# Kernel optimization log

Hardware: AMD Instinct MI355X
Metric: run time of the kernel (lower is better)

Reference implementation:

```python
import jax, jax.numpy as jnp
import numpy as np

B, H, W = 8, 512, 512          # batch, detector grid
M_PER_B = 32768
N = B * M_PER_B
C_IN, C_OUT, RED = 64, 128, 4
EPS = 1e-5


def setup_inputs() -> dict:
    key = jax.random.key(0)
    ks = jax.random.split(key, 8)
    # unique active-site indices per batch (permutation of flat grid cells)
    rng = np.random.default_rng(0)
    rows = []
    for b in range(B):
        flat = rng.permutation(H * W)[:M_PER_B]
        y, x = flat // W, flat % W
        rows.append(np.stack([np.full(M_PER_B, b), y, x], axis=1))
    indices = jnp.asarray(np.concatenate(rows, 0), dtype=jnp.int32)  # [N,3]

    feats = jax.random.normal(ks[0], (N, C_IN), jnp.float32)
    s1 = 1.0 / np.sqrt(9 * C_IN)
    s2 = 1.0 / np.sqrt(9 * C_OUT)
    return {
        "feats": feats,
        "indices": indices,
        "bn1_g": jnp.ones((C_IN,), jnp.float32),
        "bn1_b": jnp.zeros((C_IN,), jnp.float32),
        "w1": jax.random.normal(ks[1], (9, C_IN, C_OUT), jnp.float32) * s1,
        "bn2_g": jnp.ones((C_OUT,), jnp.float32),
        "bn2_b": jnp.zeros((C_OUT,), jnp.float32),
        "w2": jax.random.normal(ks[2], (9, C_OUT, C_OUT), jnp.float32) * s2,
        "fc1_w": jax.random.normal(ks[3], (C_OUT // RED, C_OUT), jnp.float32) / np.sqrt(C_OUT),
        "fc1_b": jnp.zeros((C_OUT // RED,), jnp.float32),
        "fc2_w": jax.random.normal(ks[4], (C_OUT, C_OUT // RED), jnp.float32) / np.sqrt(C_OUT // RED),
        "fc2_b": jnp.zeros((C_OUT,), jnp.float32),
        "w_skip": jax.random.normal(ks[5], (C_IN, C_OUT), jnp.float32) / np.sqrt(C_IN),
    }


def build_rulebook(indices):
    """Neighbor point-ids for each 3x3 offset. Returns ids [N,9], mask [N,9]."""
    n = indices.shape[0]
    b, y, x = indices[:, 0], indices[:, 1], indices[:, 2]
    grid = jnp.full((B, H, W), -1, jnp.int32).at[b, y, x].set(
        jnp.arange(n, dtype=jnp.int32))
    ids, masks = [], []
    for dy in (-1, 0, 1):
        for dx in (-1, 0, 1):
            ny, nx = y + dy, x + dx
            inb = (ny >= 0) & (ny < H) & (nx >= 0) & (nx < W)
            nid = grid[b, jnp.clip(ny, 0, H - 1), jnp.clip(nx, 0, W - 1)]
            m = inb & (nid >= 0)
            ids.append(jnp.where(m, nid, 0))
            masks.append(m)
    return jnp.stack(ids, 1), jnp.stack(masks, 1)


def subm_conv(f, nbr_ids, nbr_mask, w):
    """Submanifold 3x3 conv: gather-GEMM-scatter over active sites."""
    out = jnp.zeros((f.shape[0], w.shape[2]), f.dtype)
    for k in range(w.shape[0]):  # fixed 9 kernel offsets
        g = jnp.where(nbr_mask[:, k:k + 1], f[nbr_ids[:, k]], 0.0)
        out = out + g @ w[k]
    return out


def batchnorm(x, g, b):
    m = jnp.mean(x, 0)
    v = jnp.var(x, 0)  # biased, matches torch BN training normalization
    return (x - m) * jax.lax.rsqrt(v + EPS) * g + b


def reference(feats, indices, bn1_g, bn1_b, w1, bn2_g, bn2_b, w2,
              fc1_w, fc1_b, fc2_w, fc2_b, w_skip):
    nbr_ids, nbr_mask = build_rulebook(indices)  # shared indice_key rulebook
    bidx = indices[:, 0]

    out = jax.nn.relu(batchnorm(feats, bn1_g, bn1_b))
    out = subm_conv(out, nbr_ids, nbr_mask, w1)
    out = jax.nn.relu(batchnorm(out, bn2_g, bn2_b))
    out = subm_conv(out, nbr_ids, nbr_mask, w2)

    # SE: scatter-mean pool per event, FC-ReLU-FC-Sigmoid, per-site rescale
    pooled = jax.ops.segment_sum(out, bidx, num_segments=B)
    counts = jax.ops.segment_sum(jnp.ones((out.shape[0], 1), out.dtype), bidx,
                                 num_segments=B)
    pooled = pooled / jnp.clip(counts, 1.0, None)
    se = jax.nn.sigmoid(jax.nn.relu(pooled @ fc1_w.T + fc1_b) @ fc2_w.T + fc2_b)
    out = out * se[bidx]

    identity = feats @ w_skip  # 1x1 subm conv skip (in_ch != out_ch)
    return out + identity
```

## Files before the change

### kernel.cpp

```cpp
#include <hip/hip_runtime.h>
#include <math.h>

#define NPTS 262144
#define BB 8
#define HH 512
#define WW 512
#define EPSV 1e-5f

typedef short short8v __attribute__((ext_vector_type(8)));
typedef short short4v __attribute__((ext_vector_type(4)));
typedef float float4v __attribute__((ext_vector_type(4)));
typedef unsigned short ushort;
typedef ushort ushort8v __attribute__((ext_vector_type(8)));

static __device__ __forceinline__ ushort f2bf(float f) {
  union { float f; unsigned u; } v;
  v.f = f;
  unsigned r = v.u + 0x7fffu + ((v.u >> 16) & 1u);
  return (ushort)(r >> 16);
}

static __device__ __forceinline__ float bf2f(ushort h) {
  union { unsigned u; float f; } v;
  v.u = ((unsigned)h) << 16;
  return v.f;
}


__global__ __launch_bounds__(256) void k_scatter(const int* __restrict__ idx,
                                                 int* __restrict__ grid) {
  int i = blockIdx.x * 256 + threadIdx.x;
  int b = idx[i * 3 + 0], y = idx[i * 3 + 1], x = idx[i * 3 + 2];
  grid[(b * HH + y) * WW + x] = i;
}

__global__ __launch_bounds__(256) void k_rulebook(const int* __restrict__ idx,
                                                  const int* __restrict__ grid,
                                                  int* __restrict__ nbr) {
  int i = blockIdx.x * 256 + threadIdx.x;
  int b = idx[i * 3 + 0], y = idx[i * 3 + 1], x = idx[i * 3 + 2];
  int t = 0;
  #pragma unroll
  for (int dy = -1; dy <= 1; ++dy) {
    #pragma unroll
    for (int dx = -1; dx <= 1; ++dx) {
      int ny = y + dy, nx = x + dx;
      int v = -1;
      if (ny >= 0 && ny < HH && nx >= 0 && nx < WW)
        v = grid[(b * HH + ny) * WW + nx];
      nbr[i * 9 + t] = v;
      ++t;
    }
  }
}


__global__ __launch_bounds__(256) void k_stats64(const float* __restrict__ x,
                                                 float* __restrict__ sum,
                                                 float* __restrict__ ssum) {
  __shared__ float red_s[4][64];
  __shared__ float red_q[4][64];
  const int tid = threadIdx.x;
  const int lane = tid & 63;
  const int wave = tid >> 6;
  const int c4 = lane & 15;
  const int rq = lane >> 4;
  long long base = (long long)blockIdx.x * 256;
  float s0 = 0.f, s1 = 0.f, s2 = 0.f, s3 = 0.f;
  float q0 = 0.f, q1 = 0.f, q2 = 0.f, q3 = 0.f;
  for (int r = wave * 4 + rq; r < 256; r += 16) {
    float4 v = *(const float4*)(x + (base + r) * 64 + c4 * 4);
    s0 += v.x; s1 += v.y; s2 += v.z; s3 += v.w;
    q0 += v.x * v.x; q1 += v.y * v.y; q2 += v.z * v.z; q3 += v.w * v.w;
  }
  s0 += __shfl_xor(s0, 16, 64); s0 += __shfl_xor(s0, 32, 64);
  s1 += __shfl_xor(s1, 16, 64); s1 += __shfl_xor(s1, 32, 64);
  s2 += __shfl_xor(s2, 16, 64); s2 += __shfl_xor(s2, 32, 64);
  s3 += __shfl_xor(s3, 16, 64); s3 += __shfl_xor(s3, 32, 64);
  q0 += __shfl_xor(q0, 16, 64); q0 += __shfl_xor(q0, 32, 64);
  q1 += __shfl_xor(q1, 16, 64); q1 += __shfl_xor(q1, 32, 64);
  q2 += __shfl_xor(q2, 16, 64); q2 += __shfl_xor(q2, 32, 64);
  q3 += __shfl_xor(q3, 16, 64); q3 += __shfl_xor(q3, 32, 64);
  if (rq == 0) {
    red_s[wave][c4 * 4 + 0] = s0; red_s[wave][c4 * 4 + 1] = s1;
    red_s[wave][c4 * 4 + 2] = s2; red_s[wave][c4 * 4 + 3] = s3;
    red_q[wave][c4 * 4 + 0] = q0; red_q[wave][c4 * 4 + 1] = q1;
    red_q[wave][c4 * 4 + 2] = q2; red_q[wave][c4 * 4 + 3] = q3;
  }
  __syncthreads();
  if (tid < 64) {
    float ts = red_s[0][tid] + red_s[1][tid] + red_s[2][tid] + red_s[3][tid];
    float tq = red_q[0][tid] + red_q[1][tid] + red_q[2][tid] + red_q[3][tid];
    atomicAdd(&sum[tid], ts);
    atomicAdd(&ssum[tid], tq);
  }
}

template <int CI>
__global__ void k_finalize(const float* __restrict__ sum, const float* __restrict__ ssum,
                           const float* __restrict__ gam, const float* __restrict__ bet,
                           float* __restrict__ sc, float* __restrict__ sh) {
  int c = threadIdx.x;
  if (c < CI) {
    float m = sum[c] * (1.f / NPTS);
    float v = ssum[c] * (1.f / NPTS) - m * m;
    float s = gam[c] * rsqrtf(v + EPSV);
    sc[c] = s;
    sh[c] = bet[c] - m * s;
  }
}


__global__ __launch_bounds__(256) void k_wprep(const float* __restrict__ w,
                                               ushort* __restrict__ wt,
                                               int taps, int ci) {
  int i = blockIdx.x * 256 + threadIdx.x;
  int total = taps * ci * 128;
  if (i < total) {
    int t = i / (ci * 128);
    int rem = i - t * ci * 128;
    int c = rem >> 7;
    int o = rem & 127;
    wt[((size_t)t * 128 + o) * ci + c] = f2bf(w[i]);
  }
}


template <typename SrcT, typename DstT, int CI, int TAPS, bool ACT, int EPI>
__global__ __launch_bounds__(256) void k_conv(const SrcT* __restrict__ src,
                                              const float* __restrict__ scale,
                                              const float* __restrict__ shift,
                                              const int* __restrict__ nbr,
                                              const ushort* __restrict__ wt,
                                              DstT* __restrict__ dst,
                                              float* __restrict__ e0,
                                              float* __restrict__ e1) {
  constexpr int SA = CI + 8;
  __shared__ ushort As[128 * SA];
  __shared__ ushort Bs[128 * SA];
  __shared__ float s_sc[CI], s_sh[CI];

  const int tid = threadIdx.x;
  const int base = blockIdx.x * 128;
  const int lane = tid & 63;
  const int wave = tid >> 6;
  const int wm = wave & 1, wn = wave >> 1;
  const int m_base = wm * 64, n_base = wn * 64;
  const int fm = lane & 15;
  const int fq = lane >> 4;

  if constexpr (ACT) {
    for (int c = tid; c < CI; c += 256) {
      s_sc[c] = scale[c];
      s_sh[c] = shift[c];
    }
  }
  __syncthreads();

  float4v acc[4][4];
  #pragma unroll
  for (int i = 0; i < 4; ++i)
    #pragma unroll
    for (int j = 0; j < 4; ++j) acc[i][j] = (float4v){0.f, 0.f, 0.f, 0.f};

  const int srow_i = tid >> 1;
  const int shalf = tid & 1;
  const int c0 = shalf * (CI / 2);

  for (int k = 0; k < TAPS; ++k) {
    if (k) __syncthreads();

    int nid;
    if constexpr (TAPS == 1) {
      nid = base + srow_i;
    } else {
      nid = nbr[(base + srow_i) * 9 + k];
    }
    ushort* arow = &As[srow_i * SA + c0];
    if (nid >= 0) {
      const SrcT* gsrc = src + (size_t)nid * CI + c0;
      if constexpr (sizeof(SrcT) == 4) {
        #pragma unroll
        for (int j = 0; j < CI / 2; j += 4) {
          float4 v = *(const float4*)((const float*)gsrc + j);
          if constexpr (ACT) {
            int c = c0 + j;
            v.x = fmaxf(v.x * s_sc[c + 0] + s_sh[c + 0], 0.f);
            v.y = fmaxf(v.y * s_sc[c + 1] + s_sh[c + 1], 0.f);
            v.z = fmaxf(v.z * s_sc[c + 2] + s_sh[c + 2], 0.f);
            v.w = fmaxf(v.w * s_sc[c + 3] + s_sh[c + 3], 0.f);
          }
          short4v o = {(short)f2bf(v.x), (short)f2bf(v.y), (short)f2bf(v.z), (short)f2bf(v.w)};
          *(short4v*)(arow + j) = o;
        }
      } else {
        #pragma unroll
        for (int j = 0; j < CI / 2; j += 8) {
          ushort8v raw = *(const ushort8v*)((const ushort*)gsrc + j);
          short8v o;
          #pragma unroll
          for (int e = 0; e < 8; ++e) {
            float f = bf2f(raw[e]);
            if constexpr (ACT) {
              int c = c0 + j + e;
              f = fmaxf(f * s_sc[c] + s_sh[c], 0.f);
            }
            o[e] = (short)f2bf(f);
          }
          *(short8v*)(arow + j) = o;
        }
      }
    } else {
      #pragma unroll
      for (int j = 0; j < CI / 2; j += 4)
        *(short4v*)(arow + j) = (short4v){0, 0, 0, 0};
    }

    {
      const ushort* wrow = wt + ((size_t)k * 128 + srow_i) * CI + c0;
      ushort* brow = &Bs[srow_i * SA + c0];
      #pragma unroll
      for (int j = 0; j < CI / 2; j += 8)
        *(uint4*)(brow + j) = *(const uint4*)(wrow + j);
    }
    __syncthreads();

    #pragma unroll
    for (int kc = 0; kc < CI / 32; ++kc) {
      short8v af[4], bf[4];
      #pragma unroll
      for (int mi = 0; mi < 4; ++mi)
        af[mi] = *(const short8v*)(&As[(m_base + mi * 16 + fm) * SA + kc * 32 + fq * 8]);
      #pragma unroll
      for (int ni = 0; ni < 4; ++ni)
        bf[ni] = *(const short8v*)(&Bs[(n_base + ni * 16 + fm) * SA + kc * 32 + fq * 8]);
      #pragma unroll
      for (int mi = 0; mi < 4; ++mi)
        #pragma unroll
        for (int ni = 0; ni < 4; ++ni)
          acc[mi][ni] = __builtin_amdgcn_mfma_f32_16x16x32_bf16(af[mi], bf[ni], acc[mi][ni], 0, 0, 0);
    }
  }

  float es[4], ess[4];
  if constexpr (EPI) {
    #pragma unroll
    for (int ni = 0; ni < 4; ++ni) { es[ni] = 0.f; ess[ni] = 0.f; }
  }
  #pragma unroll
  for (int mi = 0; mi < 4; ++mi) {
    #pragma unroll
    for (int ni = 0; ni < 4; ++ni) {
      int pt = base + m_base + mi * 16 + fq * 4;
      int co = n_base + ni * 16 + fm;
      float4v c = acc[mi][ni];
      #pragma unroll
      for (int r = 0; r < 4; ++r) {
        if constexpr (sizeof(DstT) == 4) {
          ((float*)dst)[(size_t)(pt + r) * 128 + co] = c[r];
          if constexpr (EPI == 2) es[ni] += c[r];
        } else {
          ushort h = f2bf(c[r]);
          ((ushort*)dst)[(size_t)(pt + r) * 128 + co] = h;
          if constexpr (EPI == 1) {
            float v = bf2f(h);
            es[ni] += v;
            ess[ni] += v * v;
          }
        }
      }
    }
  }

  if constexpr (EPI) {
    #pragma unroll
    for (int ni = 0; ni < 4; ++ni) {
      float s = es[ni];
      s += __shfl_xor(s, 16, 64);
      s += __shfl_xor(s, 32, 64);
      float q = 0.f;
      if constexpr (EPI == 1) {
        q = ess[ni];
        q += __shfl_xor(q, 16, 64);
        q += __shfl_xor(q, 32, 64);
      }
      if (fq == 0) {
        int co = n_base + ni * 16 + fm;
        if constexpr (EPI == 1) {
          atomicAdd(&e0[co], s);
          atomicAdd(&e1[co], q);
        } else {
          int b = base >> 15;
          atomicAdd(&e0[b * 128 + co], s);
        }
      }
    }
  }
}


__global__ __launch_bounds__(256) void k_se(const float* __restrict__ pooled,
                                            const float* __restrict__ fc1w,
                                            const float* __restrict__ fc1b,
                                            const float* __restrict__ fc2w,
                                            const float* __restrict__ fc2b,
                                            float* __restrict__ se) {
  __shared__ float h[8][32];
  int tid = threadIdx.x;
  int b = tid >> 5, j = tid & 31;
  float s = fc1b[j];
  for (int c = 0; c < 128; ++c)
    s += pooled[b * 128 + c] * (1.f / 32768.f) * fc1w[j * 128 + c];
  h[b][j] = fmaxf(s, 0.f);
  __syncthreads();
  for (int t = tid; t < 1024; t += 256) {
    int bb = t >> 7, c = t & 127;
    float s2 = fc2b[c];
    #pragma unroll
    for (int jj = 0; jj < 32; ++jj) s2 += h[bb][jj] * fc2w[c * 32 + jj];
    se[t] = 1.f / (1.f + expf(-s2));
  }
}

__global__ __launch_bounds__(256) void k_final(float* __restrict__ out,
                                               const ushort* __restrict__ id,
                                               const float* __restrict__ se) {
  long long i = ((long long)blockIdx.x * 256 + threadIdx.x) * 4;
  int co = (int)(i & 127);
  long long rowi = i >> 7;
  int b = (int)(rowi >> 15);
  float4 o = *(const float4*)(out + i);
  ushort dh[4];
  *(uint2*)dh = *(const uint2*)(id + i);
  float4 s = *(const float4*)(se + b * 128 + co);
  o.x = o.x * s.x + bf2f(dh[0]);
  o.y = o.y * s.y + bf2f(dh[1]);
  o.z = o.z * s.z + bf2f(dh[2]);
  o.w = o.w * s.w + bf2f(dh[3]);
  *(float4*)(out + i) = o;
}


extern "C" void kernel_launch(void* const* d_in, const int* in_sizes, int n_in,
                              void* d_out, int out_size, void* d_ws, size_t ws_size,
                              hipStream_t stream) {
  const float* feats = (const float*)d_in[0];
  const int* indices = (const int*)d_in[1];
  const float* bn1_g = (const float*)d_in[2];
  const float* bn1_b = (const float*)d_in[3];
  const float* w1    = (const float*)d_in[4];
  const float* bn2_g = (const float*)d_in[5];
  const float* bn2_b = (const float*)d_in[6];
  const float* w2    = (const float*)d_in[7];
  const float* fc1w  = (const float*)d_in[8];
  const float* fc1b  = (const float*)d_in[9];
  const float* fc2w  = (const float*)d_in[10];
  const float* fc2b  = (const float*)d_in[11];
  const float* wskip = (const float*)d_in[12];
  float* out = (float*)d_out;

  char* p = (char*)d_ws;
  int* nbr = (int*)p;       p += (size_t)NPTS * 9 * 4;
  float* stats = (float*)p; p += 4096 * 4;
  ushort* wt1 = (ushort*)p; p += (size_t)9 * 128 * 64 * 2;
  ushort* wt2 = (ushort*)p; p += (size_t)9 * 128 * 128 * 2;
  ushort* wts = (ushort*)p; p += (size_t)128 * 64 * 2;
  p = (char*)(((size_t)p + 255) & ~(size_t)255);
  int* grid_i = (int*)p;
  ushort* out1 = (ushort*)p;

  float* sum1 = stats, *ss1 = stats + 64, *sc1 = stats + 128, *sh1 = stats + 192;
  float* sum2 = stats + 256, *ss2 = stats + 384, *sc2 = stats + 512, *sh2 = stats + 640;
  float* pooled = stats + 768;
  float* se = stats + 1792;

  hipMemsetAsync(grid_i, 0xFF, (size_t)BB * HH * WW * 4, stream);
  hipMemsetAsync(stats, 0, 4096 * 4, stream);

  k_scatter<<<NPTS / 256, 256, 0, stream>>>(indices, grid_i);
  k_rulebook<<<NPTS / 256, 256, 0, stream>>>(indices, grid_i, nbr);

  k_wprep<<<(9 * 64 * 128 + 255) / 256, 256, 0, stream>>>(w1, wt1, 9, 64);
  k_wprep<<<(9 * 128 * 128 + 255) / 256, 256, 0, stream>>>(w2, wt2, 9, 128);
  k_wprep<<<(64 * 128 + 255) / 256, 256, 0, stream>>>(wskip, wts, 1, 64);

  k_stats64<<<NPTS / 256, 256, 0, stream>>>(feats, sum1, ss1);
  k_finalize<64><<<1, 64, 0, stream>>>(sum1, ss1, bn1_g, bn1_b, sc1, sh1);

  k_conv<float, ushort, 64, 9, true, 1><<<NPTS / 128, 256, 0, stream>>>(
      feats, sc1, sh1, nbr, wt1, out1, sum2, ss2);

  k_finalize<128><<<1, 128, 0, stream>>>(sum2, ss2, bn2_g, bn2_b, sc2, sh2);

  k_conv<ushort, float, 128, 9, true, 2><<<NPTS / 128, 256, 0, stream>>>(
      out1, sc2, sh2, nbr, wt2, out, pooled, nullptr);

  k_conv<float, ushort, 64, 1, false, 0><<<NPTS / 128, 256, 0, stream>>>(
      feats, nullptr, nullptr, nullptr, wts, out1, nullptr, nullptr);

  k_se<<<1, 256, 0, stream>>>(pooled, fc1w, fc1b, fc2w, fc2b, se);
  k_final<<<NPTS * 128 / 1024, 256, 0, stream>>>(out, out1, se);
}
```

Before: 675.7 us.

## Pre-normalize activations to bf16 and gather directly into MFMA fragments

Adds standalone BN+ReLU kernels that write pre-normalized bf16 activations, so the convolution no longer normalizes and converts each neighbor on every tap. A new direct-gather conv kernel loads A fragments from global memory straight into MFMA registers, with no LDS staging and no __syncthreads. The rulebook is transposed to tap-major so neighbor-id loads are coalesced. This costs two extra elementwise passes and scattered 16-byte gathers that may miss cache. A fallback path keeps the old kernels when the workspace is too small.

```diff
diff --git a/kernel.cpp b/kernel.cpp
--- a/kernel.cpp
+++ b/kernel.cpp
@@ -36,7 +36,7 @@
 
 __global__ __launch_bounds__(256) void k_rulebook(const int* __restrict__ idx,
                                                   const int* __restrict__ grid,
-                                                  int* __restrict__ nbr) {
+                                                  int* __restrict__ nbrT) {
   int i = blockIdx.x * 256 + threadIdx.x;
   int b = idx[i * 3 + 0], y = idx[i * 3 + 1], x = idx[i * 3 + 2];
   int t = 0;
@@ -48,7 +48,7 @@
       int v = -1;
       if (ny >= 0 && ny < HH && nx >= 0 && nx < WW)
         v = grid[(b * HH + ny) * WW + nx];
-      nbr[i * 9 + t] = v;
+      nbrT[(size_t)t * NPTS + i] = v;
       ++t;
     }
   }
@@ -111,6 +111,53 @@
 }
 
 
+__global__ __launch_bounds__(256) void k_norm1(const float* __restrict__ x,
+                                               const float* __restrict__ sc,
+                                               const float* __restrict__ sh,
+                                               ushort* __restrict__ y) {
+  long long i = ((long long)blockIdx.x * 256 + threadIdx.x) * 8;
+  int c = (int)(i & 63);
+  float4 a = *(const float4*)(x + i);
+  float4 b = *(const float4*)(x + i + 4);
+  float4 s0 = *(const float4*)(sc + c);
+  float4 s1 = *(const float4*)(sc + c + 4);
+  float4 h0 = *(const float4*)(sh + c);
+  float4 h1 = *(const float4*)(sh + c + 4);
+  ushort8v o;
+  o[0] = f2bf(fmaxf(a.x * s0.x + h0.x, 0.f));
+  o[1] = f2bf(fmaxf(a.y * s0.y + h0.y, 0.f));
+  o[2] = f2bf(fmaxf(a.z * s0.z + h0.z, 0.f));
+  o[3] = f2bf(fmaxf(a.w * s0.w + h0.w, 0.f));
+  o[4] = f2bf(fmaxf(b.x * s1.x + h1.x, 0.f));
+  o[5] = f2bf(fmaxf(b.y * s1.y + h1.y, 0.f));
+  o[6] = f2bf(fmaxf(b.z * s1.z + h1.z, 0.f));
+  o[7] = f2bf(fmaxf(b.w * s1.w + h1.w, 0.f));
+  *(ushort8v*)(y + i) = o;
+}
+
+__global__ __launch_bounds__(256) void k_norm2(ushort* __restrict__ x,
+                                               const float* __restrict__ sc,
+                                               const float* __restrict__ sh) {
+  long long i = ((long long)blockIdx.x * 256 + threadIdx.x) * 8;
+  int c = (int)(i & 127);
+  ushort8v v = *(const ushort8v*)(x + i);
+  float4 s0 = *(const float4*)(sc + c);
+  float4 s1 = *(const float4*)(sc + c + 4);
+  float4 h0 = *(const float4*)(sh + c);
+  float4 h1 = *(const float4*)(sh + c + 4);
+  ushort8v o;
+  o[0] = f2bf(fmaxf(bf2f(v[0]) * s0.x + h0.x, 0.f));
+  o[1] = f2bf(fmaxf(bf2f(v[1]) * s0.y + h0.y, 0.f));
+  o[2] = f2bf(fmaxf(bf2f(v[2]) * s0.z + h0.z, 0.f));
+  o[3] = f2bf(fmaxf(bf2f(v[3]) * s0.w + h0.w, 0.f));
+  o[4] = f2bf(fmaxf(bf2f(v[4]) * s1.x + h1.x, 0.f));
+  o[5] = f2bf(fmaxf(bf2f(v[5]) * s1.y + h1.y, 0.f));
+  o[6] = f2bf(fmaxf(bf2f(v[6]) * s1.z + h1.z, 0.f));
+  o[7] = f2bf(fmaxf(bf2f(v[7]) * s1.w + h1.w, 0.f));
+  *(ushort8v*)(x + i) = o;
+}
+
+
 __global__ __launch_bounds__(256) void k_wprep(const float* __restrict__ w,
                                                ushort* __restrict__ wt,
                                                int taps, int ci) {
@@ -126,11 +173,121 @@
 }
 
 
+template <int CI, typename DstT, int EPI>
+__global__ __launch_bounds__(256) void k_convd(const ushort* __restrict__ src,
+                                               const int* __restrict__ nbrT,
+                                               const ushort* __restrict__ wt,
+                                               DstT* __restrict__ dst,
+                                               float* __restrict__ e0,
+                                               float* __restrict__ e1) {
+  const int tid = threadIdx.x;
+  const int base = blockIdx.x * 128;
+  const int lane = tid & 63;
+  const int wave = tid >> 6;
+  const int wm = wave & 1, wn = wave >> 1;
+  const int m_base = wm * 64, n_base = wn * 64;
+  const int fm = lane & 15;
+  const int fq = lane >> 4;
+  const int koff = fq * 8;
+
+  float4v acc[4][4];
+  #pragma unroll
+  for (int i = 0; i < 4; ++i)
+    #pragma unroll
+    for (int j = 0; j < 4; ++j) acc[i][j] = (float4v){0.f, 0.f, 0.f, 0.f};
+
+  const int* nrow = nbrT + base + m_base + fm;
+
+  for (int k = 0; k < 9; ++k) {
+    int nid0 = nrow[(size_t)k * NPTS + 0];
+    int nid1 = nrow[(size_t)k * NPTS + 16];
+    int nid2 = nrow[(size_t)k * NPTS + 32];
+    int nid3 = nrow[(size_t)k * NPTS + 48];
+    const ushort* wrow = wt + ((size_t)k * 128 + n_base + fm) * CI + koff;
+    #pragma unroll
+    for (int kc = 0; kc < CI / 32; ++kc) {
+      short8v bfr[4];
+      #pragma unroll
+      for (int ni = 0; ni < 4; ++ni)
+        bfr[ni] = *(const short8v*)(wrow + ni * 16 * CI + kc * 32);
+      const short8v z = {0, 0, 0, 0, 0, 0, 0, 0};
+      short8v a0 = (nid0 >= 0) ? *(const short8v*)(src + (size_t)nid0 * CI + kc * 32 + koff) : z;
+      short8v a1 = (nid1 >= 0) ? *(const short8v*)(src + (size_t)nid1 * CI + kc * 32 + koff) : z;
+      short8v a2 = (nid2 >= 0) ? *(const short8v*)(src + (size_t)nid2 * CI + kc * 32 + koff) : z;
+      short8v a3 = (nid3 >= 0) ? *(const short8v*)(src + (size_t)nid3 * CI + kc * 32 + koff) : z;
+      #pragma unroll
+      for (int ni = 0; ni < 4; ++ni) acc[0][ni] = __builtin_amdgcn_mfma_f32_16x16x32_bf16(a0, bfr[ni], acc[0][ni], 0, 0, 0);
+      #pragma unroll
+      for (int ni = 0; ni < 4; ++ni) acc[1][ni] = __builtin_amdgcn_mfma_f32_16x16x32_bf16(a1, bfr[ni], acc[1][ni], 0, 0, 0);
+      #pragma unroll
+      for (int ni = 0; ni < 4; ++ni) acc[2][ni] = __builtin_amdgcn_mfma_f32_16x16x32_bf16(a2, bfr[ni], acc[2][ni], 0, 0, 0);
+      #pragma unroll
+      for (int ni = 0; ni < 4; ++ni) acc[3][ni] = __builtin_amdgcn_mfma_f32_16x16x32_bf16(a3, bfr[ni], acc[3][ni], 0, 0, 0);
+    }
+  }
+
+  float es[4], ess[4];
+  if constexpr (EPI) {
+    #pragma unroll
+    for (int ni = 0; ni < 4; ++ni) { es[ni] = 0.f; ess[ni] = 0.f; }
+  }
+  #pragma unroll
+  for (int mi = 0; mi < 4; ++mi) {
+    #pragma unroll
+    for (int ni = 0; ni < 4; ++ni) {
+      int pt = base + m_base + mi * 16 + fq * 4;
+      int co = n_base + ni * 16 + fm;
+      float4v c = acc[mi][ni];
+      #pragma unroll
+      for (int r = 0; r < 4; ++r) {
+        if constexpr (sizeof(DstT) == 4) {
+          ((float*)dst)[(size_t)(pt + r) * 128 + co] = c[r];
+          if constexpr (EPI == 2) es[ni] += c[r];
+        } else {
+          ushort h = f2bf(c[r]);
+          ((ushort*)dst)[(size_t)(pt + r) * 128 + co] = h;
+          if constexpr (EPI == 1) {
+            float v = bf2f(h);
+            es[ni] += v;
+            ess[ni] += v * v;
+          }
+        }
+      }
+    }
+  }
+
+  if constexpr (EPI) {
+    #pragma unroll
+    for (int ni = 0; ni < 4; ++ni) {
+      float s = es[ni];
+      s += __shfl_xor(s, 16, 64);
+      s += __shfl_xor(s, 32, 64);
+      float q = 0.f;
+      if constexpr (EPI == 1) {
+        q = ess[ni];
+        q += __shfl_xor(q, 16, 64);
+        q += __shfl_xor(q, 32, 64);
+      }
+      if (fq == 0) {
+        int co = n_base + ni * 16 + fm;
+        if constexpr (EPI == 1) {
+          atomicAdd(&e0[co], s);
+          atomicAdd(&e1[co], q);
+        } else {
+          int b = base >> 15;
+          atomicAdd(&e0[b * 128 + co], s);
+        }
+      }
+    }
+  }
+}
+
+
 template <typename SrcT, typename DstT, int CI, int TAPS, bool ACT, int EPI>
 __global__ __launch_bounds__(256) void k_conv(const SrcT* __restrict__ src,
                                               const float* __restrict__ scale,
                                               const float* __restrict__ shift,
-                                              const int* __restrict__ nbr,
+                                              const int* __restrict__ nbrT,
                                               const ushort* __restrict__ wt,
                                               DstT* __restrict__ dst,
                                               float* __restrict__ e0,
@@ -174,7 +331,7 @@
     if constexpr (TAPS == 1) {
       nid = base + srow_i;
     } else {
-      nid = nbr[(base + srow_i) * 9 + k];
+      nid = nbrT[(size_t)k * NPTS + base + srow_i];
     }
     ushort* arow = &As[srow_i * SA + c0];
     if (nid >= 0) {
@@ -360,44 +517,84 @@
   float* out = (float*)d_out;
 
   char* p = (char*)d_ws;
-  int* nbr = (int*)p;       p += (size_t)NPTS * 9 * 4;
+  int* nbrT = (int*)p;      p += (size_t)NPTS * 9 * 4;
   float* stats = (float*)p; p += 4096 * 4;
   ushort* wt1 = (ushort*)p; p += (size_t)9 * 128 * 64 * 2;
   ushort* wt2 = (ushort*)p; p += (size_t)9 * 128 * 128 * 2;
   ushort* wts = (ushort*)p; p += (size_t)128 * 64 * 2;
   p = (char*)(((size_t)p + 255) & ~(size_t)255);
-  int* grid_i = (int*)p;
-  ushort* out1 = (ushort*)p;
 
   float* sum1 = stats, *ss1 = stats + 64, *sc1 = stats + 128, *sh1 = stats + 192;
   float* sum2 = stats + 256, *ss2 = stats + 384, *sc2 = stats + 512, *sh2 = stats + 640;
   float* pooled = stats + 768;
   float* se = stats + 1792;
 
-  hipMemsetAsync(grid_i, 0xFF, (size_t)BB * HH * WW * 4, stream);
+  size_t fixed = (size_t)(p - (char*)d_ws);
+  size_t need_new = fixed + (size_t)NPTS * 64 * 2 + (size_t)NPTS * 128 * 2;
+  bool big = ws_size >= need_new;
+
   hipMemsetAsync(stats, 0, 4096 * 4, stream);
 
-  k_scatter<<<NPTS / 256, 256, 0, stream>>>(indices, grid_i);
-  k_rulebook<<<NPTS / 256, 256, 0, stream>>>(indices, grid_i, nbr);
-
-  k_wprep<<<(9 * 64 * 128 + 255) / 256, 256, 0, stream>>>(w1, wt1, 9, 64);
-  k_wprep<<<(9 * 128 * 128 + 255) / 256, 256, 0, stream>>>(w2, wt2, 9, 128);
-  k_wprep<<<(64 * 128 + 255) / 256, 256, 0, stream>>>(wskip, wts, 1, 64);
-
-  k_stats64<<<NPTS / 256, 256, 0, stream>>>(feats, sum1, ss1);
-  k_finalize<64><<<1, 64, 0, stream>>>(sum1, ss1, bn1_g, bn1_b, sc1, sh1);
-
-  k_conv<float, ushort, 64, 9, true, 1><<<NPTS / 128, 256, 0, stream>>>(
-      feats, sc1, sh1, nbr, wt1, out1, sum2, ss2);
-
-  k_finalize<128><<<1, 128, 0, stream>>>(sum2, ss2, bn2_g, bn2_b, sc2, sh2);
-
-  k_conv<ushort, float, 128, 9, true, 2><<<NPTS / 128, 256, 0, stream>>>(
-      out1, sc2, sh2, nbr, wt2, out, pooled, nullptr);
-
-  k_conv<float, ushort, 64, 1, false, 0><<<NPTS / 128, 256, 0, stream>>>(
-      feats, nullptr, nullptr, nullptr, wts, out1, nullptr, nullptr);
-
-  k_se<<<1, 256, 0, stream>>>(pooled, fc1w, fc1b, fc2w, fc2b, se);
-  k_final<<<NPTS * 128 / 1024, 256, 0, stream>>>(out, out1, se);
-}
+  if (big) {
+    int* grid_i = (int*)p;
+    ushort* featsn = (ushort*)p;
+    ushort* out1 = (ushort*)(p + (size_t)NPTS * 64 * 2);
+
+    hipMemsetAsync(grid_i, 0xFF, (size_t)BB * HH * WW * 4, stream);
+    k_scatter<<<NPTS / 256, 256, 0, stream>>>(indices, grid_i);
+    k_rulebook<<<NPTS / 256, 256, 0, stream>>>(indices, grid_i, nbrT);
+
+    k_wprep<<<(9 * 64 * 128 + 255) / 256, 256, 0, stream>>>(w1, wt1, 9, 64);
+    k_wprep<<<(9 * 128 * 128 + 255) / 256, 256, 0, stream>>>(w2, wt2, 9, 128);
+    k_wprep<<<(64 * 128 + 255) / 256, 256, 0, stream>>>(wskip, wts, 1, 64);
+
+    k_stats64<<<NPTS / 256, 256, 0, stream>>>(feats, sum1, ss1);
+    k_finalize<64><<<1, 64, 0, stream>>>(sum1, ss1, bn1_g, bn1_b, sc1, sh1);
+
+    k_norm1<<<NPTS * 64 / 8 / 256, 256, 0, stream>>>(feats, sc1, sh1, featsn);
+
+    k_convd<64, ushort, 1><<<NPTS / 128, 256, 0, stream>>>(
+        featsn, nbrT, wt1, out1, sum2, ss2);
+
+    k_finalize<128><<<1, 128, 0, stream>>>(sum2, ss2, bn2_g, bn2_b, sc2, sh2);
+
+    k_norm2<<<NPTS * 128 / 8 / 256, 256, 0, stream>>>(out1, sc2, sh2);
+
+    k_convd<128, float, 2><<<NPTS / 128, 256, 0, stream>>>(
+        out1, nbrT, wt2, out, pooled, nullptr);
+
+    k_conv<float, ushort, 64, 1, false, 0><<<NPTS / 128, 256, 0, stream>>>(
+        feats, nullptr, nullptr, nullptr, wts, out1, nullptr, nullptr);
+
+    k_se<<<1, 256, 0, stream>>>(pooled, fc1w, fc1b, fc2w, fc2b, se);
+    k_final<<<NPTS * 128 / 1024, 256, 0, stream>>>(out, out1, se);
+  } else {
+    int* grid_i = (int*)p;
+    ushort* out1 = (ushort*)p;
+
+    hipMemsetAsync(grid_i, 0xFF, (size_t)BB * HH * WW * 4, stream);
+    k_scatter<<<NPTS / 256, 256, 0, stream>>>(indices, grid_i);
+    k_rulebook<<<NPTS / 256, 256, 0, stream>>>(indices, grid_i, nbrT);
+
+    k_wprep<<<(9 * 64 * 128 + 255) / 256, 256, 0, stream>>>(w1, wt1, 9, 64);
+    k_wprep<<<(9 * 128 * 128 + 255) / 256, 256, 0, stream>>>(w2, wt2, 9, 128);
+    k_wprep<<<(64 * 128 + 255) / 256, 256, 0, stream>>>(wskip, wts, 1, 64);
+
+    k_stats64<<<NPTS / 256, 256, 0, stream>>>(feats, sum1, ss1);
+    k_finalize<64><<<1, 64, 0, stream>>>(sum1, ss1, bn1_g, bn1_b, sc1, sh1);
+
+    k_conv<float, ushort, 64, 9, true, 1><<<NPTS / 128, 256, 0, stream>>>(
+        feats, sc1, sh1, nbrT, wt1, out1, sum2, ss2);
+
+    k_finalize<128><<<1, 128, 0, stream>>>(sum2, ss2, bn2_g, bn2_b, sc2, sh2);
+
+    k_conv<ushort, float, 128, 9, true, 2><<<NPTS / 128, 256, 0, stream>>>(
+        out1, sc2, sh2, nbrT, wt2, out, pooled, nullptr);
+
+    k_conv<float, ushort, 64, 1, false, 0><<<NPTS / 128, 256, 0, stream>>>(
+        feats, nullptr, nullptr, nullptr, wts, out1, nullptr, nullptr);
+
+    k_se<<<1, 256, 0, stream>>>(pooled, fc1w, fc1b, fc2w, fc2b, se);
+    k_final<<<NPTS * 128 / 1024, 256, 0, stream>>>(out, out1, se);
+  }
+}
```

Measured after the change: 710.0 us. 5.1% more time.
